# Kernel optimization log

Measured on AMD Instinct MI355X. Metric: run time of the kernel, lower is better.

Reference implementation:

```python
import jax, jax.numpy as jnp
import numpy as np
from functools import partial

D_MODEL = 256
D_STATE = 16
DT_RANK = 16  # ceil(d_model/16)
LN_EPS = 1e-5


def setup_inputs() -> dict:
    key = jax.random.key(0)
    ks = jax.random.split(key, 8)
    B, L, d, N, r = 16, 2048, D_MODEL, D_STATE, DT_RANK
    x = jax.random.normal(ks[0], (B, L, d), dtype=jnp.float32)
    # LayerNorm params
    ln_w = jnp.ones((d,), jnp.float32)
    ln_b = jnp.zeros((d,), jnp.float32)
    # S6 params
    x_proj_w = jax.random.normal(ks[1], (d, r + 2 * N), jnp.float32) / np.sqrt(d)
    dt_proj_w = jax.random.normal(ks[2], (r, d), jnp.float32) / np.sqrt(r)
    dt_proj_b = jax.random.uniform(ks[3], (d,), jnp.float32, -4.0, -2.0)  # softplus -> small dt
    A_log = jnp.log(jnp.tile(jnp.arange(1, N + 1, dtype=jnp.float32), (d, 1)))  # (d, N)
    D_skip = jnp.ones((d,), jnp.float32)
    # GLU params
    glu_w = jax.random.normal(ks[4], (d, 2 * d), jnp.float32) / np.sqrt(d)
    glu_b = jnp.zeros((2 * d,), jnp.float32)
    return {"x": x, "ln_w": ln_w, "ln_b": ln_b, "x_proj_w": x_proj_w,
            "dt_proj_w": dt_proj_w, "dt_proj_b": dt_proj_b, "A_log": A_log,
            "D_skip": D_skip, "glu_w": glu_w, "glu_b": glu_b}


def _layernorm(x, w, b):
    mu = jnp.mean(x, -1, keepdims=True)
    var = jnp.mean(jnp.square(x - mu), -1, keepdims=True)
    return (x - mu) * jax.lax.rsqrt(var + LN_EPS) * w + b


def _s6(x, x_proj_w, dt_proj_w, dt_proj_b, A_log, D_skip):
    # x: (B, L, d) selective scan (S6)
    Bsz, L, d = x.shape
    N = A_log.shape[1]
    A = -jnp.exp(A_log)                       # (d, N)
    dbl = x @ x_proj_w                        # (B, L, r+2N)
    dt, Bm, Cm = jnp.split(dbl, [DT_RANK, DT_RANK + N], axis=-1)
    delta = jax.nn.softplus(dt @ dt_proj_w + dt_proj_b)  # (B, L, d)

    def step(h, inp):
        d_t, b_t, c_t, x_t = inp              # (B,d),(B,N),(B,N),(B,d)
        dA = jnp.exp(d_t[..., None] * A)      # (B, d, N)
        h = dA * h + (d_t * x_t)[..., None] * b_t[:, None, :]
        y = jnp.einsum('bdn,bn->bd', h, c_t)
        return h, y

    h0 = jnp.zeros((Bsz, d, N), x.dtype)
    xs = (jnp.swapaxes(delta, 0, 1), jnp.swapaxes(Bm, 0, 1),
          jnp.swapaxes(Cm, 0, 1), jnp.swapaxes(x, 0, 1))
    _, ys = jax.lax.scan(step, h0, xs)        # ys: (L, B, d)
    return jnp.swapaxes(ys, 0, 1) + x * D_skip


def _glu(x, w, b):
    d = x.shape[-1]
    out = x @ w + b
    return out[..., :d] * jax.nn.sigmoid(out[..., d:])


@jax.jit
def reference(x, ln_w, ln_b, x_proj_w, dt_proj_w, dt_proj_b, A_log, D_skip, glu_w, glu_b):
    skip = x
    h = _layernorm(x, ln_w, ln_b)
    h = _s6(h, x_proj_w, dt_proj_w, dt_proj_b, A_log, D_skip)
    h = jax.nn.gelu(h, approximate=False)     # dropout = identity (eval)
    h = _glu(h, glu_w, glu_b)
    return h + skip
```

## Files before the change

kernel.cpp:

```cpp
#include <hip/hip_runtime.h>
#include <hip/hip_bf16.h>

#define BB 16
#define LL 2048
#define DD 256
#define NN 16
#define RR 16
#define CH 64
#define LC (LL/CH)

static __device__ __forceinline__ float bf2f(unsigned short u) {
    return __uint_as_float(((unsigned)u) << 16);
}
static __device__ __forceinline__ unsigned short f2bf(float f) {
    unsigned u = __float_as_uint(f);
    u += 0x7FFFu + ((u >> 16) & 1u);
    return (unsigned short)(u >> 16);
}

typedef __attribute__((ext_vector_type(8))) short bf16x8;
typedef __attribute__((ext_vector_type(4))) short bf16x4;
typedef __attribute__((ext_vector_type(4))) float f32x4;

static __device__ __forceinline__ void pow_tree(float E, float* e) {
    e[0] = E;
    e[1] = E * E;
    e[2] = e[1] * E;
    e[3] = e[1] * e[1];
    e[4] = e[3] * e[0];  e[5] = e[3] * e[1];  e[6] = e[3] * e[2];  e[7] = e[3] * e[3];
    e[8] = e[7] * e[0];  e[9] = e[7] * e[1];  e[10] = e[7] * e[2]; e[11] = e[7] * e[3];
    e[12] = e[7] * e[4]; e[13] = e[7] * e[5]; e[14] = e[7] * e[6]; e[15] = e[7] * e[7];
}

__global__ __launch_bounds__(256) void k_prep_wx(
    const float* __restrict__ xw, unsigned short* __restrict__ Wxt)
{
    const int idx = blockIdx.x * 256 + threadIdx.x;
    const int n  = idx >> 6;
    const int k0 = (idx & 63) * 4;
    #pragma unroll
    for (int i = 0; i < 4; ++i) {
        float v = (n < 48) ? xw[(size_t)(k0 + i) * 48 + n] : 0.f;
        Wxt[(size_t)n * DD + k0 + i] = f2bf(v);
    }
}

__global__ __launch_bounds__(256) void k_transpose(
    const float* __restrict__ W, unsigned short* __restrict__ Wt)
{
    __shared__ unsigned short s[32][33];
    const int bx = blockIdx.x;
    const int by = blockIdx.y;
    const int t = threadIdx.x;
    const int r = t >> 5, cc = t & 31;
    #pragma unroll
    for (int i = 0; i < 4; ++i)
        s[r + 8*i][cc] = f2bf(W[(size_t)(by*32 + r + 8*i)*512 + bx*32 + cc]);
    __syncthreads();
    #pragma unroll
    for (int i = 0; i < 4; ++i)
        Wt[(size_t)(bx*32 + r + 8*i)*256 + by*32 + cc] = s[cc][r + 8*i];
}

__global__ __launch_bounds__(256) void k_ln_fused(
    const float* __restrict__ x,
    const float* __restrict__ ln_w,
    const float* __restrict__ ln_b,
    const unsigned short* __restrict__ Wxt,
    const float* __restrict__ dtw,
    const float* __restrict__ dtb,
    unsigned short* __restrict__ xln,
    unsigned short* __restrict__ delta,
    float* __restrict__ Bv,
    float* __restrict__ Cv)
{
    const int t = threadIdx.x;
    const int m0 = blockIdx.x * 32;
    const int row = t >> 3, seg = t & 7;
    const int grow = m0 + row;

    __shared__ unsigned short As[32][264];
    __shared__ float sdt[32][20];
    __shared__ float sdtw[16*256];
    __shared__ float slnw[256], slnb[256], sdtb[256];

    {
        const int tt = t & 63;
        if (t < 64)       *(float4*)&slnw[tt*4] = *(const float4*)&ln_w[tt*4];
        else if (t < 128) *(float4*)&slnb[tt*4] = *(const float4*)&ln_b[tt*4];
        else if (t < 192) *(float4*)&sdtb[tt*4] = *(const float4*)&dtb[tt*4];
        #pragma unroll
        for (int k = 0; k < 4; ++k)
            *(float4*)&sdtw[(k*256 + t)*4] = *(const float4*)&dtw[(k*256 + t)*4];
    }

    float v[32];
    #pragma unroll
    for (int i = 0; i < 8; ++i)
        *(float4*)&v[i*4] = *(const float4*)(x + (size_t)grow*DD + i*32 + seg*4);

    float s = 0.f, q = 0.f;
    #pragma unroll
    for (int i = 0; i < 32; ++i) { s += v[i]; q = fmaf(v[i], v[i], q); }
    #pragma unroll
    for (int o = 1; o < 8; o <<= 1) {
        s += __shfl_xor(s, o);
        q += __shfl_xor(q, o);
    }
    const float mu = s * (1.f/DD);
    const float rs = rsqrtf(q * (1.f/DD) - mu*mu + 1e-5f);
    __syncthreads();

    unsigned short o16[32];
    #pragma unroll
    for (int i = 0; i < 8; ++i) {
        const int c = i*32 + seg*4;
        const float4 wv = *(const float4*)&slnw[c];
        const float4 bv = *(const float4*)&slnb[c];
        o16[i*4+0] = f2bf((v[i*4+0]-mu)*rs*wv.x + bv.x);
        o16[i*4+1] = f2bf((v[i*4+1]-mu)*rs*wv.y + bv.y);
        o16[i*4+2] = f2bf((v[i*4+2]-mu)*rs*wv.z + bv.z);
        o16[i*4+3] = f2bf((v[i*4+3]-mu)*rs*wv.w + bv.w);
    }
    #pragma unroll
    for (int i = 0; i < 8; ++i) {
        const int c = i*32 + seg*4;
        *(bf16x4*)&xln[(size_t)grow*DD + c] = *(bf16x4*)&o16[i*4];
        *(bf16x4*)&As[row][c]               = *(bf16x4*)&o16[i*4];
    }
    __syncthreads();

    const int w = t >> 6, lane = t & 63;
    const int cl = lane & 15, rq = lane >> 4;
    const int mh = (w & 1) * 16;
    const int nh = (w >> 1) * 32;
    f32x4 acc0 = {0.f,0.f,0.f,0.f}, acc1 = {0.f,0.f,0.f,0.f};
    #pragma unroll
    for (int k0 = 0; k0 < 256; k0 += 32) {
        const bf16x8 a  = *(const bf16x8*)&As[mh + cl][k0 + rq*8];
        const bf16x8 b0 = *(const bf16x8*)&Wxt[(size_t)(nh + cl)*DD + k0 + rq*8];
        acc0 = __builtin_amdgcn_mfma_f32_16x16x32_bf16(a, b0, acc0, 0, 0, 0);
        if (w < 2) {
            const bf16x8 b1 = *(const bf16x8*)&Wxt[(size_t)(nh + 16 + cl)*DD + k0 + rq*8];
            acc1 = __builtin_amdgcn_mfma_f32_16x16x32_bf16(a, b1, acc1, 0, 0, 0);
        }
    }
    if (w < 2) {
        #pragma unroll
        for (int r = 0; r < 4; ++r) {
            sdt[mh + rq*4 + r][cl] = acc0[r];
            Bv[(size_t)(m0 + mh + rq*4 + r)*NN + cl] = acc1[r];
        }
    } else {
        #pragma unroll
        for (int r = 0; r < 4; ++r)
            Cv[(size_t)(m0 + mh + rq*4 + r)*NN + cl] = acc0[r];
    }
    __syncthreads();

    float dt[16];
    #pragma unroll
    for (int j = 0; j < 16; ++j) dt[j] = sdt[row][j];
    #pragma unroll
    for (int i = 0; i < 8; ++i) {
        const int c = i*32 + seg*4;
        float4 a4 = *(const float4*)&sdtb[c];
        #pragma unroll
        for (int j = 0; j < 16; ++j) {
            const float4 w4 = *(const float4*)&sdtw[j*256 + c];
            a4.x = fmaf(dt[j], w4.x, a4.x);
            a4.y = fmaf(dt[j], w4.y, a4.y);
            a4.z = fmaf(dt[j], w4.z, a4.z);
            a4.w = fmaf(dt[j], w4.w, a4.w);
        }
        unsigned short d16[4];
        #pragma unroll
        for (int jj = 0; jj < 4; ++jj) {
            const float ac = (&a4.x)[jj];
            const float sp = (ac > 15.f) ? ac
                : 0.69314718f * log2f(1.f + exp2f(ac * 1.44269504f));
            d16[jj] = f2bf(sp);
        }
        *(bf16x4*)&delta[(size_t)grow*DD + c] = *(bf16x4*)&d16[0];
    }
}

template<bool FAST>
__device__ __forceinline__ void scan1_impl(
    const unsigned short (*sD)[264], const unsigned short (*sX)[264],
    const float (*sB)[16],
    const float* al, int d, float* h, float* dsum)
{
    #pragma unroll 4
    for (int l = 0; l < LC; ++l) {
        const float dl = bf2f(sD[l][d]);
        const float xl = bf2f(sX[l][d]);
        const float dx = dl * xl;
        *dsum += dl;
        float e[NN];
        if (FAST) pow_tree(exp2f(al[0]*dl), e);
        else {
            #pragma unroll
            for (int n = 0; n < NN; ++n) e[n] = exp2f(al[n]*dl);
        }
        #pragma unroll
        for (int n = 0; n < NN; ++n)
            h[n] = fmaf(e[n], h[n], dx * sB[l][n]);
    }
}

__global__ __launch_bounds__(256) void k_scan1(
    const unsigned short* __restrict__ delta,
    const unsigned short* __restrict__ xln,
    const float* __restrict__ Bv,
    const float* __restrict__ A_log,
    float* __restrict__ S, float* __restrict__ Dsum)
{
    const int blk = blockIdx.x;
    const int c = blk & (CH-1);
    const int b = blk >> 6;
    const int d = threadIdx.x;
    const int l0 = c * LC;
    __shared__ unsigned short sD[LC][264];
    __shared__ unsigned short sX[LC][264];
    __shared__ float sB[LC][16];

    {
        const int sr = d >> 3, sc = (d & 7) * 32;
        const size_t gbase = ((size_t)b*LL + l0 + sr)*DD + sc;
        #pragma unroll
        for (int i = 0; i < 4; ++i) {
            *(bf16x8*)&sD[sr][sc + i*8] = *(const bf16x8*)&delta[gbase + i*8];
            *(bf16x8*)&sX[sr][sc + i*8] = *(const bf16x8*)&xln  [gbase + i*8];
        }
        if (d < 128) {
            const int l = d >> 2, qq = (d & 3) * 4;
            *(float4*)&sB[l][qq] = *(const float4*)&Bv[((size_t)b*LL + l0 + l)*NN + qq];
        }
    }
    float al[NN];
    bool fast = true;
    #pragma unroll
    for (int n = 0; n < NN; ++n) {
        al[n] = -expf(A_log[d*NN + n]) * 1.44269504f;
        fast = fast && (fabsf(al[n] - (n+1)*al[0]) <= 1e-3f*fabsf(al[n]) + 1e-6f);
    }
    float h[NN];
    #pragma unroll
    for (int n = 0; n < NN; ++n) h[n] = 0.f;
    float dsum = 0.f;
    __syncthreads();
    if (fast) scan1_impl<true >(sD, sX, sB, al, d, h, &dsum);
    else      scan1_impl<false>(sD, sX, sB, al, d, h, &dsum);
    const size_t o = (size_t)blk * NN * DD + d;
    #pragma unroll
    for (int n = 0; n < NN; ++n) S[o + n*DD] = h[n];
    Dsum[(size_t)blk*DD + d] = dsum;
}

__global__ __launch_bounds__(256) void k_combine(
    const float* __restrict__ S, const float* __restrict__ Dsum,
    const float* __restrict__ A_log, float* __restrict__ Hin)
{
    const int bi = blockIdx.x;
    const int d = threadIdx.x;
    const int n = bi & 15;
    const int b = bi >> 4;
    const float al = -expf(A_log[d*NN + n]) * 1.44269504f;
    float h = 0.f;
    for (int c0 = 0; c0 < CH; c0 += 8) {
        float ds8[8], s8[8];
        #pragma unroll
        for (int i = 0; i < 8; ++i) {
            const size_t blk = (size_t)b*CH + c0 + i;
            ds8[i] = Dsum[blk*DD + d];
            s8[i]  = S[(blk*NN + n)*DD + d];
        }
        #pragma unroll
        for (int i = 0; i < 8; ++i) {
            const size_t blk = (size_t)b*CH + c0 + i;
            Hin[(blk*NN + n)*DD + d] = h;
            h = fmaf(exp2f(al * ds8[i]), h, s8[i]);
        }
    }
}

template<bool FAST>
__device__ __forceinline__ void scan2_impl(
    const unsigned short (*sD)[264], const unsigned short (*sX)[264],
    const float (*sB)[16], const float (*sC)[16],
    const float* al, int d, float* h, float dsk,
    size_t gout, unsigned short* __restrict__ g)
{
    #pragma unroll 4
    for (int l = 0; l < LC; ++l) {
        const float dl = bf2f(sD[l][d]);
        const float xl = bf2f(sX[l][d]);
        const float dx = dl * xl;
        float e[NN];
        if (FAST) pow_tree(exp2f(al[0]*dl), e);
        else {
            #pragma unroll
            for (int n = 0; n < NN; ++n) e[n] = exp2f(al[n]*dl);
        }
        float y = 0.f;
        #pragma unroll
        for (int n = 0; n < NN; ++n) {
            h[n] = fmaf(e[n], h[n], dx * sB[l][n]);
            y = fmaf(h[n], sC[l][n], y);
        }
        const float vv = y + xl * dsk;
        const float u  = 0.7978845608f * (vv + 0.044715f*vv*vv*vv);
        const float t2 = exp2f(2.8853900818f * u);
        const float th = 1.f - 2.f/(t2 + 1.f);
        g[gout + (size_t)l*DD] = f2bf(0.5f * vv * (1.f + th));
    }
}

__global__ __launch_bounds__(256) void k_scan2(
    const unsigned short* __restrict__ delta,
    const unsigned short* __restrict__ xln,
    const float* __restrict__ Bv,
    const float* __restrict__ Cv,
    const float* __restrict__ A_log,
    const float* __restrict__ Hin,
    const float* __restrict__ Dskip,
    unsigned short* __restrict__ g)
{
    const int blk = blockIdx.x;
    const int c = blk & (CH-1);
    const int b = blk >> 6;
    const int d = threadIdx.x;
    const int l0 = c * LC;
    __shared__ unsigned short sD[LC][264];
    __shared__ unsigned short sX[LC][264];
    __shared__ float sB[LC][16], sC[LC][16];

    {
        const int sr = d >> 3, sc = (d & 7) * 32;
        const size_t gbase = ((size_t)b*LL + l0 + sr)*DD + sc;
        #pragma unroll
        for (int i = 0; i < 4; ++i) {
            *(bf16x8*)&sD[sr][sc + i*8] = *(const bf16x8*)&delta[gbase + i*8];
            *(bf16x8*)&sX[sr][sc + i*8] = *(const bf16x8*)&xln  [gbase + i*8];
        }
        if (d < 128) {
            const int l = d >> 2, qq = (d & 3) * 4;
            *(float4*)&sB[l][qq] = *(const float4*)&Bv[((size_t)b*LL + l0 + l)*NN + qq];
        } else {
            const int dd = d - 128;
            const int l = dd >> 2, qq = (dd & 3) * 4;
            *(float4*)&sC[l][qq] = *(const float4*)&Cv[((size_t)b*LL + l0 + l)*NN + qq];
        }
    }
    float al[NN];
    bool fast = true;
    #pragma unroll
    for (int n = 0; n < NN; ++n) {
        al[n] = -expf(A_log[d*NN + n]) * 1.44269504f;
        fast = fast && (fabsf(al[n] - (n+1)*al[0]) <= 1e-3f*fabsf(al[n]) + 1e-6f);
    }
    float h[NN];
    const size_t ob = (size_t)blk * NN * DD + d;
    #pragma unroll
    for (int n = 0; n < NN; ++n) h[n] = Hin[ob + n*DD];
    const float dsk = Dskip[d];
    __syncthreads();
    const size_t gout = ((size_t)b*LL + l0)*DD + d;
    if (fast) scan2_impl<true >(sD, sX, sB, sC, al, d, h, dsk, gout, g);
    else      scan2_impl<false>(sD, sX, sB, sC, al, d, h, dsk, gout, g);
}

__global__ __launch_bounds__(256) void k_glu(
    const unsigned short* __restrict__ g,
    const unsigned short* __restrict__ Wt,
    const float* __restrict__ gb,
    const float* __restrict__ x,
    float* __restrict__ out)
{
    __shared__ unsigned short As[64][40];
    __shared__ unsigned short Bl[64][40];
    __shared__ unsigned short Bh[64][40];
    const int n0 = blockIdx.x * 64;
    const int m0 = blockIdx.y * 64;
    const int t = threadIdx.x;
    const int w = t >> 6, lane = t & 63;
    const int r = t >> 2, q = t & 3;
    const int cl = lane & 15, rq = lane >> 4;
    f32x4 accL[4], accH[4];
    const f32x4 zz = {0.f, 0.f, 0.f, 0.f};
    #pragma unroll
    for (int nf = 0; nf < 4; ++nf) { accL[nf] = zz; accH[nf] = zz; }

    for (int k0 = 0; k0 < 256; k0 += 32) {
        *(bf16x8*)(&As[r][q*8]) = *(const bf16x8*)(&g [(size_t)(m0+r)*DD + k0 + q*8]);
        *(bf16x8*)(&Bl[r][q*8]) = *(const bf16x8*)(&Wt[(size_t)(n0+r)*DD + k0 + q*8]);
        *(bf16x8*)(&Bh[r][q*8]) = *(const bf16x8*)(&Wt[(size_t)(n0+256+r)*DD + k0 + q*8]);
        __syncthreads();
        const bf16x8 a = *(const bf16x8*)(&As[w*16 + cl][rq*8]);
        #pragma unroll
        for (int nf = 0; nf < 4; ++nf) {
            const bf16x8 bl = *(const bf16x8*)(&Bl[nf*16 + cl][rq*8]);
            const bf16x8 bh = *(const bf16x8*)(&Bh[nf*16 + cl][rq*8]);
            accL[nf] = __builtin_amdgcn_mfma_f32_16x16x32_bf16(a, bl, accL[nf], 0, 0, 0);
            accH[nf] = __builtin_amdgcn_mfma_f32_16x16x32_bf16(a, bh, accH[nf], 0, 0, 0);
        }
        __syncthreads();
    }
    #pragma unroll
    for (int nf = 0; nf < 4; ++nf) {
        const int j = n0 + nf*16 + cl;
        const float bL = gb[j];
        const float bH = gb[j + 256];
        #pragma unroll
        for (int rr = 0; rr < 4; ++rr) {
            const int m = m0 + w*16 + rq*4 + rr;
            const float lo = accL[nf][rr] + bL;
            const float hi = accH[nf][rr] + bH;
            const float sg = 1.f / (1.f + exp2f(-1.44269504f * hi));
            out[(size_t)m*DD + j] = lo * sg + x[(size_t)m*DD + j];
        }
    }
}

extern "C" void kernel_launch(void* const* d_in, const int* in_sizes, int n_in,
                              void* d_out, int out_size, void* d_ws, size_t ws_size,
                              hipStream_t stream)
{
    const float* x    = (const float*)d_in[0];
    const float* ln_w = (const float*)d_in[1];
    const float* ln_b = (const float*)d_in[2];
    const float* xpw  = (const float*)d_in[3];
    const float* dtw  = (const float*)d_in[4];
    const float* dtb  = (const float*)d_in[5];
    const float* alog = (const float*)d_in[6];
    const float* dsk  = (const float*)d_in[7];
    const float* gw   = (const float*)d_in[8];
    const float* gb   = (const float*)d_in[9];
    float* out = (float*)d_out;

    char* ws = (char*)d_ws;
    size_t off = 0;
    auto alloc = [&](size_t bytes) {
        char* p = ws + off; off += (bytes + 255) & ~(size_t)255; return p;
    };
    unsigned short* xln   = (unsigned short*)alloc((size_t)BB*LL*DD*2);
    unsigned short* delta = (unsigned short*)alloc((size_t)BB*LL*DD*2);
    float*          Bvp   = (float*)         alloc((size_t)BB*LL*NN*4);
    float*          Cvp   = (float*)         alloc((size_t)BB*LL*NN*4);
    float*          S     = (float*)         alloc((size_t)BB*CH*NN*DD*4);
    float*          Dsum  = (float*)         alloc((size_t)BB*CH*DD*4);
    float*          Hin   = (float*)         alloc((size_t)BB*CH*NN*DD*4);
    unsigned short* Wt    = (unsigned short*)alloc((size_t)512*256*2);
    unsigned short* Wxt   = (unsigned short*)alloc((size_t)64*256*2);
    unsigned short* g     = delta;

    k_prep_wx<<<16, 256, 0, stream>>>(xpw, Wxt);
    k_transpose<<<dim3(16, 8), 256, 0, stream>>>(gw, Wt);
    k_ln_fused<<<1024, 256, 0, stream>>>(x, ln_w, ln_b, Wxt, dtw, dtb, xln, delta, Bvp, Cvp);
    k_scan1<<<BB*CH, 256, 0, stream>>>(delta, xln, Bvp, alog, S, Dsum);
    k_combine<<<256, 256, 0, stream>>>(S, Dsum, alog, Hin);
    k_scan2<<<BB*CH, 256, 0, stream>>>(delta, xln, Bvp, Cvp, alog, Hin, dsk, g);
    k_glu<<<dim3(4, 512), 256, 0, stream>>>(g, Wt, gb, x, out);
}
```

Before: 117.7 us.

## Fuse LayerNorm/projection kernel into chunk scan pass one

Merges the LayerNorm + x_proj + dt_proj kernel with the first chunked scan pass, so each block normalizes its 32-row chunk, computes dt/B/C via MFMA, and scans immediately from shared memory. The delta projection is now computed per thread-channel inside the scan loop, which removes one kernel launch and the re-read of delta, xln and B from global memory. It also splits the y reduction in scan2 into four partial accumulators to shorten the dependency chain. The cost is heavier per-thread work in the scan loop and higher register pressure.

```diff
diff --git a/kernel.cpp b/kernel.cpp
--- a/kernel.cpp
+++ b/kernel.cpp
@@ -62,139 +62,26 @@
         Wt[(size_t)(bx*32 + r + 8*i)*256 + by*32 + cc] = s[cc][r + 8*i];
 }
 
-__global__ __launch_bounds__(256) void k_ln_fused(
-    const float* __restrict__ x,
-    const float* __restrict__ ln_w,
-    const float* __restrict__ ln_b,
-    const unsigned short* __restrict__ Wxt,
-    const float* __restrict__ dtw,
-    const float* __restrict__ dtb,
-    unsigned short* __restrict__ xln,
+template<bool FAST>
+__device__ __forceinline__ void dt_scan1(
+    const float (*sdt)[20], const unsigned short (*As)[264],
+    const float (*sB)[16], const float* wj, float bia,
+    const float* al, int d, size_t m0,
     unsigned short* __restrict__ delta,
-    float* __restrict__ Bv,
-    float* __restrict__ Cv)
-{
-    const int t = threadIdx.x;
-    const int m0 = blockIdx.x * 32;
-    const int row = t >> 3, seg = t & 7;
-    const int grow = m0 + row;
-
-    __shared__ unsigned short As[32][264];
-    __shared__ float sdt[32][20];
-    __shared__ float sdtw[16*256];
-    __shared__ float slnw[256], slnb[256], sdtb[256];
-
-    {
-        const int tt = t & 63;
-        if (t < 64)       *(float4*)&slnw[tt*4] = *(const float4*)&ln_w[tt*4];
-        else if (t < 128) *(float4*)&slnb[tt*4] = *(const float4*)&ln_b[tt*4];
-        else if (t < 192) *(float4*)&sdtb[tt*4] = *(const float4*)&dtb[tt*4];
-        #pragma unroll
-        for (int k = 0; k < 4; ++k)
-            *(float4*)&sdtw[(k*256 + t)*4] = *(const float4*)&dtw[(k*256 + t)*4];
-    }
-
-    float v[32];
-    #pragma unroll
-    for (int i = 0; i < 8; ++i)
-        *(float4*)&v[i*4] = *(const float4*)(x + (size_t)grow*DD + i*32 + seg*4);
-
-    float s = 0.f, q = 0.f;
-    #pragma unroll
-    for (int i = 0; i < 32; ++i) { s += v[i]; q = fmaf(v[i], v[i], q); }
-    #pragma unroll
-    for (int o = 1; o < 8; o <<= 1) {
-        s += __shfl_xor(s, o);
-        q += __shfl_xor(q, o);
-    }
-    const float mu = s * (1.f/DD);
-    const float rs = rsqrtf(q * (1.f/DD) - mu*mu + 1e-5f);
-    __syncthreads();
-
-    unsigned short o16[32];
-    #pragma unroll
-    for (int i = 0; i < 8; ++i) {
-        const int c = i*32 + seg*4;
-        const float4 wv = *(const float4*)&slnw[c];
-        const float4 bv = *(const float4*)&slnb[c];
-        o16[i*4+0] = f2bf((v[i*4+0]-mu)*rs*wv.x + bv.x);
-        o16[i*4+1] = f2bf((v[i*4+1]-mu)*rs*wv.y + bv.y);
-        o16[i*4+2] = f2bf((v[i*4+2]-mu)*rs*wv.z + bv.z);
-        o16[i*4+3] = f2bf((v[i*4+3]-mu)*rs*wv.w + bv.w);
-    }
-    #pragma unroll
-    for (int i = 0; i < 8; ++i) {
-        const int c = i*32 + seg*4;
-        *(bf16x4*)&xln[(size_t)grow*DD + c] = *(bf16x4*)&o16[i*4];
-        *(bf16x4*)&As[row][c]               = *(bf16x4*)&o16[i*4];
-    }
-    __syncthreads();
-
-    const int w = t >> 6, lane = t & 63;
-    const int cl = lane & 15, rq = lane >> 4;
-    const int mh = (w & 1) * 16;
-    const int nh = (w >> 1) * 32;
-    f32x4 acc0 = {0.f,0.f,0.f,0.f}, acc1 = {0.f,0.f,0.f,0.f};
-    #pragma unroll
-    for (int k0 = 0; k0 < 256; k0 += 32) {
-        const bf16x8 a  = *(const bf16x8*)&As[mh + cl][k0 + rq*8];
-        const bf16x8 b0 = *(const bf16x8*)&Wxt[(size_t)(nh + cl)*DD + k0 + rq*8];
-        acc0 = __builtin_amdgcn_mfma_f32_16x16x32_bf16(a, b0, acc0, 0, 0, 0);
-        if (w < 2) {
-            const bf16x8 b1 = *(const bf16x8*)&Wxt[(size_t)(nh + 16 + cl)*DD + k0 + rq*8];
-            acc1 = __builtin_amdgcn_mfma_f32_16x16x32_bf16(a, b1, acc1, 0, 0, 0);
-        }
-    }
-    if (w < 2) {
-        #pragma unroll
-        for (int r = 0; r < 4; ++r) {
-            sdt[mh + rq*4 + r][cl] = acc0[r];
-            Bv[(size_t)(m0 + mh + rq*4 + r)*NN + cl] = acc1[r];
-        }
-    } else {
-        #pragma unroll
-        for (int r = 0; r < 4; ++r)
-            Cv[(size_t)(m0 + mh + rq*4 + r)*NN + cl] = acc0[r];
-    }
-    __syncthreads();
-
-    float dt[16];
-    #pragma unroll
-    for (int j = 0; j < 16; ++j) dt[j] = sdt[row][j];
-    #pragma unroll
-    for (int i = 0; i < 8; ++i) {
-        const int c = i*32 + seg*4;
-        float4 a4 = *(const float4*)&sdtb[c];
-        #pragma unroll
-        for (int j = 0; j < 16; ++j) {
-            const float4 w4 = *(const float4*)&sdtw[j*256 + c];
-            a4.x = fmaf(dt[j], w4.x, a4.x);
-            a4.y = fmaf(dt[j], w4.y, a4.y);
-            a4.z = fmaf(dt[j], w4.z, a4.z);
-            a4.w = fmaf(dt[j], w4.w, a4.w);
-        }
-        unsigned short d16[4];
-        #pragma unroll
-        for (int jj = 0; jj < 4; ++jj) {
-            const float ac = (&a4.x)[jj];
-            const float sp = (ac > 15.f) ? ac
-                : 0.69314718f * log2f(1.f + exp2f(ac * 1.44269504f));
-            d16[jj] = f2bf(sp);
-        }
-        *(bf16x4*)&delta[(size_t)grow*DD + c] = *(bf16x4*)&d16[0];
-    }
-}
-
-template<bool FAST>
-__device__ __forceinline__ void scan1_impl(
-    const unsigned short (*sD)[264], const unsigned short (*sX)[264],
-    const float (*sB)[16],
-    const float* al, int d, float* h, float* dsum)
+    float* h, float* dsum)
 {
     #pragma unroll 4
     for (int l = 0; l < LC; ++l) {
-        const float dl = bf2f(sD[l][d]);
-        const float xl = bf2f(sX[l][d]);
+        float acc = bia;
+        #pragma unroll
+        for (int j = 0; j < 16; ++j)
+            acc = fmaf(sdt[l][j], wj[j], acc);
+        const float sp = (acc > 15.f) ? acc
+            : 0.69314718f * log2f(1.f + exp2f(acc * 1.44269504f));
+        const unsigned short dbits = f2bf(sp);
+        delta[(m0 + l)*DD + d] = dbits;
+        const float dl = bf2f(dbits);
+        const float xl = bf2f(As[l][d]);
         const float dx = dl * xl;
         *dsum += dl;
         float e[NN];
@@ -209,53 +96,124 @@
     }
 }
 
-__global__ __launch_bounds__(256) void k_scan1(
-    const unsigned short* __restrict__ delta,
-    const unsigned short* __restrict__ xln,
-    const float* __restrict__ Bv,
+__global__ __launch_bounds__(256) void k_ln_scan1(
+    const float* __restrict__ x,
+    const float* __restrict__ ln_w,
+    const float* __restrict__ ln_b,
+    const unsigned short* __restrict__ Wxt,
+    const float* __restrict__ dtw,
+    const float* __restrict__ dtb,
     const float* __restrict__ A_log,
-    float* __restrict__ S, float* __restrict__ Dsum)
-{
+    unsigned short* __restrict__ xln,
+    unsigned short* __restrict__ delta,
+    float* __restrict__ Bv,
+    float* __restrict__ Cv,
+    float* __restrict__ S,
+    float* __restrict__ Dsum)
+{
+    const int t = threadIdx.x;
     const int blk = blockIdx.x;
-    const int c = blk & (CH-1);
-    const int b = blk >> 6;
-    const int d = threadIdx.x;
-    const int l0 = c * LC;
-    __shared__ unsigned short sD[LC][264];
-    __shared__ unsigned short sX[LC][264];
-    __shared__ float sB[LC][16];
+    const size_t m0 = (size_t)blk * 32;
+    const int row = t >> 3, seg = t & 7;
+    const size_t grow = m0 + row;
+
+    __shared__ unsigned short As[32][264];
+    __shared__ float sdt[32][20];
+    __shared__ float sB[32][16];
+    __shared__ float slnw[256], slnb[256], sdtb[256];
 
     {
-        const int sr = d >> 3, sc = (d & 7) * 32;
-        const size_t gbase = ((size_t)b*LL + l0 + sr)*DD + sc;
-        #pragma unroll
-        for (int i = 0; i < 4; ++i) {
-            *(bf16x8*)&sD[sr][sc + i*8] = *(const bf16x8*)&delta[gbase + i*8];
-            *(bf16x8*)&sX[sr][sc + i*8] = *(const bf16x8*)&xln  [gbase + i*8];
-        }
-        if (d < 128) {
-            const int l = d >> 2, qq = (d & 3) * 4;
-            *(float4*)&sB[l][qq] = *(const float4*)&Bv[((size_t)b*LL + l0 + l)*NN + qq];
-        }
-    }
+        const int tt = t & 63;
+        if (t < 64)       *(float4*)&slnw[tt*4] = *(const float4*)&ln_w[tt*4];
+        else if (t < 128) *(float4*)&slnb[tt*4] = *(const float4*)&ln_b[tt*4];
+        else if (t < 192) *(float4*)&sdtb[tt*4] = *(const float4*)&dtb[tt*4];
+    }
+
+    float wj[16];
+    #pragma unroll
+    for (int j = 0; j < 16; ++j) wj[j] = dtw[j*DD + t];
     float al[NN];
     bool fast = true;
     #pragma unroll
     for (int n = 0; n < NN; ++n) {
-        al[n] = -expf(A_log[d*NN + n]) * 1.44269504f;
+        al[n] = -expf(A_log[t*NN + n]) * 1.44269504f;
         fast = fast && (fabsf(al[n] - (n+1)*al[0]) <= 1e-3f*fabsf(al[n]) + 1e-6f);
     }
+
+    float v[32];
+    #pragma unroll
+    for (int i = 0; i < 8; ++i)
+        *(float4*)&v[i*4] = *(const float4*)(x + grow*DD + i*32 + seg*4);
+    float s = 0.f, q = 0.f;
+    #pragma unroll
+    for (int i = 0; i < 32; ++i) { s += v[i]; q = fmaf(v[i], v[i], q); }
+    #pragma unroll
+    for (int o = 1; o < 8; o <<= 1) {
+        s += __shfl_xor(s, o);
+        q += __shfl_xor(q, o);
+    }
+    const float mu = s * (1.f/DD);
+    const float rs = rsqrtf(q * (1.f/DD) - mu*mu + 1e-5f);
+    __syncthreads();
+
+    #pragma unroll
+    for (int i = 0; i < 8; ++i) {
+        const int c = i*32 + seg*4;
+        const float4 wv = *(const float4*)&slnw[c];
+        const float4 bv = *(const float4*)&slnb[c];
+        unsigned short o16[4];
+        o16[0] = f2bf((v[i*4+0]-mu)*rs*wv.x + bv.x);
+        o16[1] = f2bf((v[i*4+1]-mu)*rs*wv.y + bv.y);
+        o16[2] = f2bf((v[i*4+2]-mu)*rs*wv.z + bv.z);
+        o16[3] = f2bf((v[i*4+3]-mu)*rs*wv.w + bv.w);
+        *(bf16x4*)&xln[grow*DD + c] = *(bf16x4*)&o16[0];
+        *(bf16x4*)&As[row][c]       = *(bf16x4*)&o16[0];
+    }
+    __syncthreads();
+
+    {
+        const int w = t >> 6, lane = t & 63;
+        const int cl = lane & 15, rq = lane >> 4;
+        const int mh = (w & 1) * 16;
+        const int nh = (w >> 1) * 32;
+        f32x4 acc0 = {0.f,0.f,0.f,0.f}, acc1 = {0.f,0.f,0.f,0.f};
+        #pragma unroll
+        for (int k0 = 0; k0 < 256; k0 += 32) {
+            const bf16x8 a  = *(const bf16x8*)&As[mh + cl][k0 + rq*8];
+            const bf16x8 b0 = *(const bf16x8*)&Wxt[(size_t)(nh + cl)*DD + k0 + rq*8];
+            acc0 = __builtin_amdgcn_mfma_f32_16x16x32_bf16(a, b0, acc0, 0, 0, 0);
+            if (w < 2) {
+                const bf16x8 b1 = *(const bf16x8*)&Wxt[(size_t)(nh + 16 + cl)*DD + k0 + rq*8];
+                acc1 = __builtin_amdgcn_mfma_f32_16x16x32_bf16(a, b1, acc1, 0, 0, 0);
+            }
+        }
+        if (w < 2) {
+            #pragma unroll
+            for (int r = 0; r < 4; ++r) {
+                const int rr = mh + rq*4 + r;
+                sdt[rr][cl] = acc0[r];
+                sB[rr][cl]  = acc1[r];
+                Bv[(m0 + rr)*NN + cl] = acc1[r];
+            }
+        } else {
+            #pragma unroll
+            for (int r = 0; r < 4; ++r)
+                Cv[(m0 + mh + rq*4 + r)*NN + cl] = acc0[r];
+        }
+    }
+    __syncthreads();
+
     float h[NN];
     #pragma unroll
     for (int n = 0; n < NN; ++n) h[n] = 0.f;
     float dsum = 0.f;
-    __syncthreads();
-    if (fast) scan1_impl<true >(sD, sX, sB, al, d, h, &dsum);
-    else      scan1_impl<false>(sD, sX, sB, al, d, h, &dsum);
-    const size_t o = (size_t)blk * NN * DD + d;
+    const float bia = sdtb[t];
+    if (fast) dt_scan1<true >(sdt, As, sB, wj, bia, al, t, m0, delta, h, &dsum);
+    else      dt_scan1<false>(sdt, As, sB, wj, bia, al, t, m0, delta, h, &dsum);
+    const size_t o = (size_t)blk * NN * DD + t;
     #pragma unroll
     for (int n = 0; n < NN; ++n) S[o + n*DD] = h[n];
-    Dsum[(size_t)blk*DD + d] = dsum;
+    Dsum[(size_t)blk*DD + t] = dsum;
 }
 
 __global__ __launch_bounds__(256) void k_combine(
@@ -303,13 +261,13 @@
             #pragma unroll
             for (int n = 0; n < NN; ++n) e[n] = exp2f(al[n]*dl);
         }
-        float y = 0.f;
+        float yb[4] = {0.f, 0.f, 0.f, 0.f};
         #pragma unroll
         for (int n = 0; n < NN; ++n) {
             h[n] = fmaf(e[n], h[n], dx * sB[l][n]);
-            y = fmaf(h[n], sC[l][n], y);
-        }
-        const float vv = y + xl * dsk;
+            yb[n & 3] = fmaf(h[n], sC[l][n], yb[n & 3]);
+        }
+        const float vv = (yb[0]+yb[1]) + (yb[2]+yb[3]) + xl * dsk;
         const float u  = 0.7978845608f * (vv + 0.044715f*vv*vv*vv);
         const float t2 = exp2f(2.8853900818f * u);
         const float th = 1.f - 2.f/(t2 + 1.f);
@@ -457,8 +415,8 @@
 
     k_prep_wx<<<16, 256, 0, stream>>>(xpw, Wxt);
     k_transpose<<<dim3(16, 8), 256, 0, stream>>>(gw, Wt);
-    k_ln_fused<<<1024, 256, 0, stream>>>(x, ln_w, ln_b, Wxt, dtw, dtb, xln, delta, Bvp, Cvp);
-    k_scan1<<<BB*CH, 256, 0, stream>>>(delta, xln, Bvp, alog, S, Dsum);
+    k_ln_scan1<<<BB*CH, 256, 0, stream>>>(x, ln_w, ln_b, Wxt, dtw, dtb, alog,
+                                          xln, delta, Bvp, Cvp, S, Dsum);
     k_combine<<<256, 256, 0, stream>>>(S, Dsum, alog, Hin);
     k_scan2<<<BB*CH, 256, 0, stream>>>(delta, xln, Bvp, Cvp, alog, Hin, dsk, g);
     k_glu<<<dim3(4, 512), 256, 0, stream>>>(g, Wt, gb, x, out);
```

New measurement: 116.6 us. Within noise of the previous version (-0.9%).
